# Kernel optimization log

Measured on AMD Instinct MI355X. Metric: run time of the kernel, lower is better.

The kernel has to match this reference:

```python
import jax, jax.numpy as jnp
import numpy as np

B, S, D = 16, 2048, 128

def setup_inputs() -> dict:
    key = jax.random.key(0)
    kq, kk, kv = jax.random.split(key, 3)
    return {
        "query": jax.random.normal(kq, (B, S, D), dtype=jnp.float32),
        "key": jax.random.normal(kk, (B, S, D), dtype=jnp.float32),
        "value": jax.random.normal(kv, (B, S, D), dtype=jnp.float32),
    }

def reference(query, key, value):
    # query: (B, S2, d), key: (B, S1, d), value: (B, S1, d)
    d_k = query.shape[-1]
    scale = 1.0 / jnp.sqrt(jnp.asarray(d_k, dtype=query.dtype))
    # (B, S2, S1) attention scores
    att = jnp.einsum('bqd,bkd->bqk', query, key) * scale
    att = jax.nn.softmax(att, axis=-1)
    # (B, S2, d_v)
    return jnp.einsum('bqk,bkd->bqd', att, value)
```

## Files before the change

### kernel.cpp

```cpp
#include <hip/hip_runtime.h>

#define B_N 16
#define S_LEN 2048
#define D_DIM 128
#define NTH 32

typedef __attribute__((ext_vector_type(16))) float f32x16;
typedef __attribute__((ext_vector_type(8)))  short short8;
typedef __attribute__((ext_vector_type(4)))  int   i32x4;

static __device__ __forceinline__ unsigned short f2bf(float f) {
  unsigned u = __builtin_bit_cast(unsigned, f);
  return (unsigned short)((u + 0x7fffu + ((u >> 16) & 1u)) >> 16);
}

__global__ __launch_bounds__(256)
void prep_kernel(const float* __restrict__ K, const float* __restrict__ V,
                 unsigned short* __restrict__ Kf, unsigned short* __restrict__ Vf) {
  __shared__ unsigned short lds[32 * 132];
  const int bx = blockIdx.x;
  const int b  = bx >> 6;
  const int T  = bx & 63;
  const int t  = threadIdx.x;

  const float* Kb = K + ((size_t)b * S_LEN + T * 32) * D_DIM;
  const float* Vb = V + ((size_t)b * S_LEN + T * 32) * D_DIM;
  unsigned short* Kfb = Kf + ((size_t)(b * 64 + T) * 8) * 512;
  unsigned short* Vfb = Vf + ((size_t)(b * 64 + T) * 8) * 512;

#pragma unroll
  for (int rep = 0; rep < 2; ++rep) {
    int u    = rep * 256 + t;
    int ks   = u >> 6;
    int lane = u & 63;
    const float* src = Kb + (size_t)(lane & 31) * D_DIM + ks * 16 + (lane >> 5) * 8;
    float4 a0 = *(const float4*)(src);
    float4 a1 = *(const float4*)(src + 4);
    unsigned w0 = (unsigned)f2bf(a0.x) | ((unsigned)f2bf(a0.y) << 16);
    unsigned w1 = (unsigned)f2bf(a0.z) | ((unsigned)f2bf(a0.w) << 16);
    unsigned w2 = (unsigned)f2bf(a1.x) | ((unsigned)f2bf(a1.y) << 16);
    unsigned w3 = (unsigned)f2bf(a1.z) | ((unsigned)f2bf(a1.w) << 16);
    *(uint4*)(Kfb + (size_t)ks * 512 + lane * 8) = make_uint4(w0, w1, w2, w3);
  }

#pragma unroll
  for (int rep = 0; rep < 2; ++rep) {
    int id  = rep * 256 + t;
    int row = id >> 4;
    int c8  = (id & 15) * 8;
    float4 a0 = *(const float4*)(Vb + (size_t)row * D_DIM + c8);
    float4 a1 = *(const float4*)(Vb + (size_t)row * D_DIM + c8 + 4);
    unsigned short* d = &lds[row * 132 + c8];
    d[0] = f2bf(a0.x); d[1] = f2bf(a0.y); d[2] = f2bf(a0.z); d[3] = f2bf(a0.w);
    d[4] = f2bf(a1.x); d[5] = f2bf(a1.y); d[6] = f2bf(a1.z); d[7] = f2bf(a1.w);
  }
  __syncthreads();

#pragma unroll
  for (int rep = 0; rep < 2; ++rep) {
    int u    = rep * 256 + t;
    int f    = u >> 6;
    int lane = u & 63;
    int ks2  = f >> 2;
    int dt   = f & 3;
    int col  = dt * 32 + (lane & 31);
    int rbase = ks2 * 16 + (lane >> 5) * 8;
    unsigned w[4];
#pragma unroll
    for (int jj = 0; jj < 4; ++jj) {
      unsigned short e0 = lds[(rbase + 2 * jj) * 132 + col];
      unsigned short e1 = lds[(rbase + 2 * jj + 1) * 132 + col];
      w[jj] = (unsigned)e0 | ((unsigned)e1 << 16);
    }
    *(uint4*)(Vfb + (size_t)f * 512 + lane * 8) = make_uint4(w[0], w[1], w[2], w[3]);
  }
}

__global__ __launch_bounds__(128, 2)
void attn_kernel(const float* __restrict__ Q, const unsigned short* __restrict__ Kf,
                 const unsigned short* __restrict__ Vf, float* __restrict__ O) {
  __shared__ __align__(16) float smem[4160];

  const int tid  = threadIdx.x;
  const int g    = tid >> 6;
  const int lane = tid & 63;
  const int l32  = lane & 31;
  const int half = lane >> 5;

  const int i     = blockIdx.x;
  const int b     = (i & 7) * 2 + ((i >> 3) & 1);
  const int qt    = i >> 4;
  const int qbase = qt * 32;

  const float* Qb = Q + (size_t)b * S_LEN * D_DIM;
  const unsigned short* Kfb = Kf + ((size_t)(b * 64 + g * 32) * 8) * 512 + lane * 8;
  const unsigned short* Vfb = Vf + ((size_t)(b * 64 + g * 32) * 8) * 512 + lane * 8;

  short8 qa[8];
  {
    const float* qp = Qb + (size_t)(qbase + l32) * D_DIM + half * 8;
#pragma unroll
    for (int ks = 0; ks < 8; ++ks) {
      float4 a0 = *(const float4*)(qp + ks * 16);
      float4 a1 = *(const float4*)(qp + ks * 16 + 4);
      short8 f;
      f[0] = (short)f2bf(a0.x); f[1] = (short)f2bf(a0.y);
      f[2] = (short)f2bf(a0.z); f[3] = (short)f2bf(a0.w);
      f[4] = (short)f2bf(a1.x); f[5] = (short)f2bf(a1.y);
      f[6] = (short)f2bf(a1.z); f[7] = (short)f2bf(a1.w);
      qa[ks] = f;
    }
  }

  const f32x16 zf16 = {0.f,0.f,0.f,0.f,0.f,0.f,0.f,0.f,0.f,0.f,0.f,0.f,0.f,0.f,0.f,0.f};
  f32x16 oacc[4];
  float lsum = 0.f;
#pragma unroll
  for (int dt = 0; dt < 4; ++dt) oacc[dt] = zf16;

  const float SC = 0.08838834764831845f * 1.4426950408889634f;

#define LOAD_K(dst, tt)                                                            \
  _Pragma("unroll")                                                                \
  for (int ks = 0; ks < 8; ++ks)                                                   \
    dst[ks] = *(const short8*)(Kfb + (((size_t)(tt) * 8 + ks) << 9));
#define LOAD_V(dst, tt)                                                            \
  _Pragma("unroll")                                                                \
  for (int f = 0; f < 8; ++f)                                                      \
    dst[f] = *(const short8*)(Vfb + (((size_t)(tt) * 8 + f) << 9));
#define QK(kreg, saccv)                                                            \
  _Pragma("unroll")                                                                \
  for (int ks = 0; ks < 8; ++ks)                                                   \
    saccv = __builtin_amdgcn_mfma_f32_32x32x16_bf16(kreg[ks], qa[ks], saccv, 0, 0, 0);
#define SOFTMAX(saccv, pf0v, pf1v)                                                 \
  {                                                                                \
    float p_[16];                                                                  \
    _Pragma("unroll")                                                              \
    for (int reg = 0; reg < 16; ++reg) {                                           \
      p_[reg] = exp2f(saccv[reg] * SC);                                            \
      lsum += p_[reg];                                                             \
    }                                                                              \
    int dw_[8];                                                                    \
    _Pragma("unroll")                                                              \
    for (int i2 = 0; i2 < 8; ++i2)                                                 \
      asm("v_cvt_pk_bf16_f32 %0, %1, %2"                                           \
          : "=v"(dw_[i2]) : "v"(p_[2 * i2]), "v"(p_[2 * i2 + 1]));                 \
    asm("v_permlane32_swap_b32 %0, %1" : "+v"(dw_[0]), "+v"(dw_[2]));              \
    asm("v_permlane32_swap_b32 %0, %1" : "+v"(dw_[1]), "+v"(dw_[3]));              \
    asm("v_permlane32_swap_b32 %0, %1" : "+v"(dw_[4]), "+v"(dw_[6]));              \
    asm("v_permlane32_swap_b32 %0, %1" : "+v"(dw_[5]), "+v"(dw_[7]));              \
    i32x4 f0_ = {dw_[0], dw_[1], dw_[2], dw_[3]};                                  \
    i32x4 f1_ = {dw_[4], dw_[5], dw_[6], dw_[7]};                                  \
    pf0v = __builtin_bit_cast(short8, f0_);                                        \
    pf1v = __builtin_bit_cast(short8, f1_);                                        \
  }
#define PV(vreg, pf0v, pf1v)                                                       \
  _Pragma("unroll")                                                                \
  for (int dt = 0; dt < 4; ++dt) {                                                 \
    oacc[dt] = __builtin_amdgcn_mfma_f32_32x32x16_bf16(pf0v, vreg[dt],     oacc[dt], 0, 0, 0); \
    oacc[dt] = __builtin_amdgcn_mfma_f32_32x32x16_bf16(pf1v, vreg[4 + dt], oacc[dt], 0, 0, 0); \
  }

  short8 kA[8], kB[8];
  LOAD_K(kA, 0)

  for (int t = 0; t < NTH; t += 2) {
    {
      short8 vr[8];
      LOAD_V(vr, t)
      LOAD_K(kB, t + 1)
      f32x16 sacc = zf16;
      QK(kA, sacc)
      short8 pf0, pf1;
      SOFTMAX(sacc, pf0, pf1)
      PV(vr, pf0, pf1)
    }
    {
      short8 vr[8];
      LOAD_V(vr, t + 1)
      if (t + 2 < NTH) LOAD_K(kA, t + 2)
      f32x16 sacc = zf16;
      QK(kB, sacc)
      short8 pf0, pf1;
      SOFTMAX(sacc, pf0, pf1)
      PV(vr, pf0, pf1)
    }
  }
#undef LOAD_K
#undef LOAD_V
#undef QK
#undef SOFTMAX
#undef PV

  lsum += __shfl_xor(lsum, 32);

  __syncthreads();
  float* mo  = smem;
  float* ml1 = smem + 4096;
  float* ml0 = smem + 4128;
  if (g == 1) {
#pragma unroll
    for (int reg = 0; reg < 16; ++reg) {
      int row = (reg & 3) + 8 * (reg >> 2) + 4 * half;
#pragma unroll
      for (int dt = 0; dt < 4; ++dt)
        mo[row * 128 + dt * 32 + l32] = oacc[dt][reg];
    }
    if (half == 0) ml1[l32] = lsum;
  } else {
    if (half == 0) ml0[l32] = lsum;
  }
  __syncthreads();
  if (g == 0) {
    float* Ob = O + (size_t)b * S_LEN * D_DIM;
#pragma unroll
    for (int reg = 0; reg < 16; ++reg) {
      int row = (reg & 3) + 8 * (reg >> 2) + 4 * half;
      float linv = 1.f / (ml0[row] + ml1[row]);
#pragma unroll
      for (int dt = 0; dt < 4; ++dt)
        Ob[(size_t)(qbase + row) * D_DIM + dt * 32 + l32] =
            (oacc[dt][reg] + mo[row * 128 + dt * 32 + l32]) * linv;
    }
  }
}

extern "C" void kernel_launch(void* const* d_in, const int* in_sizes, int n_in,
                              void* d_out, int out_size, void* d_ws, size_t ws_size,
                              hipStream_t stream) {
  const float* Q = (const float*)d_in[0];
  const float* K = (const float*)d_in[1];
  const float* V = (const float*)d_in[2];
  float* O = (float*)d_out;
  unsigned short* Kf = (unsigned short*)d_ws;
  unsigned short* Vf = Kf + (size_t)B_N * S_LEN * D_DIM;
  prep_kernel<<<dim3(1024), dim3(256), 0, stream>>>(K, V, Kf, Vf);
  attn_kernel<<<dim3(1024), dim3(128), 0, stream>>>(Q, Kf, Vf, O);
}
```

Baseline: 142.1 us.

## Split keys four ways across waves with 64-query blocks and LDS reduction

Each block now holds 8 waves covering 64 queries: two 32-query groups, with the key sequence split into four 512-key chunks per group instead of two 1024-key halves. Partial outputs and row sums are combined in shared memory through a three-step reduction into wave group 0, which normalizes and writes the result. The aim is more waves per CU and a shorter serial key loop per wave, so latency hides better. The cost is extra LDS traffic and several block-wide barriers at the end. The row-sum accumulation in softmax is also rebalanced into a tree.

```diff
diff --git a/kernel.cpp b/kernel.cpp
--- a/kernel.cpp
+++ b/kernel.cpp
@@ -3,7 +3,7 @@
 #define B_N 16
 #define S_LEN 2048
 #define D_DIM 128
-#define NTH 32
+#define NTG 16
 
 typedef __attribute__((ext_vector_type(16))) float f32x16;
 typedef __attribute__((ext_vector_type(8)))  short short8;
@@ -76,25 +76,27 @@
   }
 }
 
-__global__ __launch_bounds__(128, 2)
+__global__ __launch_bounds__(512, 4)
 void attn_kernel(const float* __restrict__ Q, const unsigned short* __restrict__ Kf,
                  const unsigned short* __restrict__ Vf, float* __restrict__ O) {
-  __shared__ __align__(16) float smem[4160];
+  __shared__ __align__(16) float smem[8448];
 
   const int tid  = threadIdx.x;
-  const int g    = tid >> 6;
+  const int wave = tid >> 6;
+  const int g    = wave >> 1;
+  const int q2   = wave & 1;
   const int lane = tid & 63;
   const int l32  = lane & 31;
   const int half = lane >> 5;
 
   const int i     = blockIdx.x;
   const int b     = (i & 7) * 2 + ((i >> 3) & 1);
-  const int qt    = i >> 4;
-  const int qbase = qt * 32;
+  const int qtb   = i >> 4;
+  const int qbase = qtb * 64 + q2 * 32;
 
   const float* Qb = Q + (size_t)b * S_LEN * D_DIM;
-  const unsigned short* Kfb = Kf + ((size_t)(b * 64 + g * 32) * 8) * 512 + lane * 8;
-  const unsigned short* Vfb = Vf + ((size_t)(b * 64 + g * 32) * 8) * 512 + lane * 8;
+  const unsigned short* Kfb = Kf + ((size_t)(b * 64 + g * NTG) * 8) * 512 + lane * 8;
+  const unsigned short* Vfb = Vf + ((size_t)(b * 64 + g * NTG) * 8) * 512 + lane * 8;
 
   short8 qa[8];
   {
@@ -136,10 +138,12 @@
   {                                                                                \
     float p_[16];                                                                  \
     _Pragma("unroll")                                                              \
-    for (int reg = 0; reg < 16; ++reg) {                                           \
-      p_[reg] = exp2f(saccv[reg] * SC);                                            \
-      lsum += p_[reg];                                                             \
-    }                                                                              \
+    for (int reg = 0; reg < 16; ++reg) p_[reg] = exp2f(saccv[reg] * SC);           \
+    float s01_ = (p_[0] + p_[1]) + (p_[2] + p_[3]);                                \
+    float s23_ = (p_[4] + p_[5]) + (p_[6] + p_[7]);                                \
+    float s45_ = (p_[8] + p_[9]) + (p_[10] + p_[11]);                              \
+    float s67_ = (p_[12] + p_[13]) + (p_[14] + p_[15]);                            \
+    lsum += (s01_ + s23_) + (s45_ + s67_);                                         \
     int dw_[8];                                                                    \
     _Pragma("unroll")                                                              \
     for (int i2 = 0; i2 < 8; ++i2)                                                 \
@@ -164,7 +168,7 @@
   short8 kA[8], kB[8];
   LOAD_K(kA, 0)
 
-  for (int t = 0; t < NTH; t += 2) {
+  for (int t = 0; t < NTG; t += 2) {
     {
       short8 vr[8];
       LOAD_V(vr, t)
@@ -178,7 +182,7 @@
     {
       short8 vr[8];
       LOAD_V(vr, t + 1)
-      if (t + 2 < NTH) LOAD_K(kA, t + 2)
+      if (t + 2 < NTG) LOAD_K(kA, t + 2)
       f32x16 sacc = zf16;
       QK(kB, sacc)
       short8 pf0, pf1;
@@ -194,33 +198,47 @@
 
   lsum += __shfl_xor(lsum, 32);
 
+  float* mo = smem;
+  float* ml = smem + 8192;
+  if (half == 0) ml[q2 * 128 + g * 32 + l32] = lsum;
   __syncthreads();
-  float* mo  = smem;
-  float* ml1 = smem + 4096;
-  float* ml0 = smem + 4128;
-  if (g == 1) {
+#pragma unroll
+  for (int r = 1; r < 4; ++r) {
+    if (g == r) {
+#pragma unroll
+      for (int reg = 0; reg < 16; ++reg) {
+        int row = (reg & 3) + 8 * (reg >> 2) + 4 * half;
+#pragma unroll
+        for (int dt = 0; dt < 4; ++dt)
+          mo[(q2 * 32 + row) * 128 + dt * 32 + l32] = oacc[dt][reg];
+      }
+    }
+    __syncthreads();
+    if (g == 0) {
+#pragma unroll
+      for (int reg = 0; reg < 16; ++reg) {
+        int row = (reg & 3) + 8 * (reg >> 2) + 4 * half;
+#pragma unroll
+        for (int dt = 0; dt < 4; ++dt)
+          oacc[dt][reg] += mo[(q2 * 32 + row) * 128 + dt * 32 + l32];
+      }
+    }
+    __syncthreads();
+  }
+
+  if (g == 0) {
+    float* Ob = O + (size_t)b * S_LEN * D_DIM;
 #pragma unroll
     for (int reg = 0; reg < 16; ++reg) {
       int row = (reg & 3) + 8 * (reg >> 2) + 4 * half;
+      int rr = q2 * 32 + row;
+      float linv = 1.f / (ml[q2 * 128 + l32  - l32 + 0 * 32 + row] +
+                          ml[q2 * 128 + 1 * 32 + row] +
+                          ml[q2 * 128 + 2 * 32 + row] +
+                          ml[q2 * 128 + 3 * 32 + row]);
 #pragma unroll
       for (int dt = 0; dt < 4; ++dt)
-        mo[row * 128 + dt * 32 + l32] = oacc[dt][reg];
-    }
-    if (half == 0) ml1[l32] = lsum;
-  } else {
-    if (half == 0) ml0[l32] = lsum;
-  }
-  __syncthreads();
-  if (g == 0) {
-    float* Ob = O + (size_t)b * S_LEN * D_DIM;
-#pragma unroll
-    for (int reg = 0; reg < 16; ++reg) {
-      int row = (reg & 3) + 8 * (reg >> 2) + 4 * half;
-      float linv = 1.f / (ml0[row] + ml1[row]);
-#pragma unroll
-      for (int dt = 0; dt < 4; ++dt)
-        Ob[(size_t)(qbase + row) * D_DIM + dt * 32 + l32] =
-            (oacc[dt][reg] + mo[row * 128 + dt * 32 + l32]) * linv;
+        Ob[(size_t)(qtb * 64 + rr) * D_DIM + dt * 32 + l32] = oacc[dt][reg] * linv;
     }
   }
 }
@@ -235,5 +253,5 @@
   unsigned short* Kf = (unsigned short*)d_ws;
   unsigned short* Vf = Kf + (size_t)B_N * S_LEN * D_DIM;
   prep_kernel<<<dim3(1024), dim3(256), 0, stream>>>(K, V, Kf, Vf);
-  attn_kernel<<<dim3(1024), dim3(128), 0, stream>>>(Q, Kf, Vf, O);
-}
+  attn_kernel<<<dim3(512), dim3(512), 0, stream>>>(Q, Kf, Vf, O);
+}
```

Result: slower. 366.3 us (+157.8%).
